# Kernel optimization log

Hardware: AMD Instinct MI355X
Metric: run time of the kernel (lower is better)

## Reference

```python
import jax, jax.numpy as jnp
import numpy as np

C, W = 144, 9225          # channel_count, batch_width
KW, F = 10, 64            # kernel_width, fc_segment_length
H1 = 128                  # second layer out
CAT = 2 * C * F           # 18432 = C*F (fc) + (W-KW+1) (conv)


def setup_inputs() -> dict:
    key = jax.random.key(0)
    ks = jax.random.split(key, 9)
    s_fc = 1.0 / np.sqrt(W)
    s_cv = 1.0 / np.sqrt(C * KW)
    s_1 = 1.0 / np.sqrt(CAT)
    s_2 = 1.0 / np.sqrt(H1)
    return {
        "x":     jax.random.normal(ks[0], (C, W), jnp.float32),
        "Wfc":   jax.random.normal(ks[1], (C, F, W), jnp.float32) * s_fc,
        "bfc":   jax.random.normal(ks[2], (C, F), jnp.float32) * s_fc,
        "Kconv": jax.random.normal(ks[3], (C, KW), jnp.float32) * s_cv,
        "bconv": jax.random.normal(ks[4], (1,), jnp.float32) * s_cv,
        "W1":    jax.random.normal(ks[5], (H1, CAT), jnp.float32) * s_1,
        "b1":    jax.random.normal(ks[6], (H1,), jnp.float32) * s_1,
        "W2":    jax.random.normal(ks[7], (1, H1), jnp.float32) * s_2,
        "b2":    jax.random.normal(ks[8], (1,), jnp.float32) * s_2,
    }


def reference(x, Wfc, bfc, Kconv, bconv, W1, b1, W2, b2):
    # 144 per-channel Linear(W->F) fused into one batched GEMV (no ReLU on
    # these in the original forward, despite the docstring).
    fc_out = (jnp.einsum('cfw,cw->cf', Wfc, x) + bfc).reshape(-1)  # [C*F]
    # Conv2d(1,1,(C,KW)): kernel height == channel count -> 1D valid corr.
    conv = jax.lax.conv_general_dilated(
        x[None, None],            # [1,1,C,W]
        Kconv[None, None],        # [1,1,C,KW]
        window_strides=(1, 1), padding='VALID')[0, 0, 0] + bconv  # [W-KW+1]
    concatenated = jnp.concatenate([fc_out, conv])                # [CAT]
    second = jax.nn.relu(W1 @ concatenated + b1)                  # [H1]
    out = jax.nn.relu(W2 @ second + b2)                           # [1]
    return jax.nn.sigmoid(out)
```

## Files before the change

kernel.cpp:

```cpp
#include <hip/hip_runtime.h>
#include <math.h>

#define CC    144
#define WW    9225
#define KWW   10
#define FF    64
#define H1N   128
#define CONVN (WW - KWW + 1)
#define CFN   (CC * FF)
#define CATN  (CFN + CONVN)

__global__ __launch_bounds__(256) void k_front(
    const float* __restrict__ x,
    const float* __restrict__ Wfc,
    const float* __restrict__ bfc,
    const float* __restrict__ Kc,
    const float* __restrict__ bconv,
    float* __restrict__ concat)
{
    __shared__ float sm[CC * KWW];
    const int b   = blockIdx.x;
    const int tid = threadIdx.x;

    if (b < CFN) {
        const int c = b >> 6;
        const size_t base = (size_t)b * WW;
        const float* __restrict__ xr = x + (size_t)c * WW;
        const float* __restrict__ wr = Wfc + base;

        const int pro = (int)((4u - ((unsigned)(base & 3u))) & 3u);
        float acc = 0.f;
        if (tid < pro) acc += wr[tid] * xr[tid];

        const int rem  = WW - pro;
        const int nv   = rem >> 2;
        const int tail = rem & 3;
        const float4* __restrict__ wv = (const float4*)(wr + pro);

        for (int i = tid; i < nv; i += 256) {
            const float4 wq = wv[i];
            const int w0 = pro + (i << 2);
            acc += wq.x * xr[w0]     + wq.y * xr[w0 + 1]
                 + wq.z * xr[w0 + 2] + wq.w * xr[w0 + 3];
        }
        if (tid < tail) {
            const int w0 = pro + (nv << 2) + tid;
            acc += wr[w0] * xr[w0];
        }

        #pragma unroll
        for (int off = 32; off > 0; off >>= 1)
            acc += __shfl_xor(acc, off, 64);
        const int lane = tid & 63, wid = tid >> 6;
        if (lane == 0) sm[wid] = acc;
        __syncthreads();
        if (tid == 0)
            concat[b] = sm[0] + sm[1] + sm[2] + sm[3] + bfc[b];
    } else {
        for (int i = tid; i < CC * KWW; i += 256) sm[i] = Kc[i];
        __syncthreads();

        const int p = (b - CFN) * 256 + tid;
        float acc = bconv[0];
        for (int c = 0; c < CC; ++c) {
            const float* __restrict__ xr = x + (size_t)c * WW + p;
            const float* __restrict__ kr = sm + c * KWW;
            #pragma unroll
            for (int k = 0; k < KWW; ++k)
                acc = fmaf(xr[k], kr[k], acc);
        }
        concat[CFN + p] = acc;
    }
}

__global__ __launch_bounds__(256) void k_layer1(
    const float* __restrict__ W1,
    const float* __restrict__ b1,
    const float* __restrict__ concat,
    float* __restrict__ second)
{
    __shared__ float sm[4];
    const int h = blockIdx.x, tid = threadIdx.x;
    const float4* __restrict__ wr = (const float4*)(W1 + (size_t)h * CATN);
    const float4* __restrict__ cv = (const float4*)concat;

    float acc = 0.f;
    #pragma unroll 2
    for (int i = tid; i < CATN / 4; i += 256) {
        const float4 a = wr[i], q = cv[i];
        acc += a.x * q.x + a.y * q.y + a.z * q.z + a.w * q.w;
    }
    #pragma unroll
    for (int off = 32; off > 0; off >>= 1)
        acc += __shfl_xor(acc, off, 64);
    if ((tid & 63) == 0) sm[tid >> 6] = acc;
    __syncthreads();
    if (tid == 0)
        second[h] = fmaxf(sm[0] + sm[1] + sm[2] + sm[3] + b1[h], 0.f);
}

__global__ __launch_bounds__(128) void k_final(
    const float* __restrict__ second,
    const float* __restrict__ W2,
    const float* __restrict__ b2,
    float* __restrict__ out)
{
    __shared__ float sm[2];
    const int tid = threadIdx.x;
    float v = second[tid] * W2[tid];
    #pragma unroll
    for (int off = 32; off > 0; off >>= 1)
        v += __shfl_xor(v, off, 64);
    if ((tid & 63) == 0) sm[tid >> 6] = v;
    __syncthreads();
    if (tid == 0) {
        float z = sm[0] + sm[1] + b2[0];
        z = fmaxf(z, 0.f);
        out[0] = 1.f / (1.f + expf(-z));
    }
}

extern "C" void kernel_launch(void* const* d_in, const int* in_sizes, int n_in,
                              void* d_out, int out_size, void* d_ws, size_t ws_size,
                              hipStream_t stream) {
    const float* x     = (const float*)d_in[0];
    const float* Wfc   = (const float*)d_in[1];
    const float* bfc   = (const float*)d_in[2];
    const float* Kc    = (const float*)d_in[3];
    const float* bconv = (const float*)d_in[4];
    const float* W1    = (const float*)d_in[5];
    const float* b1    = (const float*)d_in[6];
    const float* W2    = (const float*)d_in[7];
    const float* b2    = (const float*)d_in[8];
    float* out = (float*)d_out;

    float* concat = (float*)d_ws;
    float* second = concat + CATN;

    k_front <<<CFN + (CONVN / 256), 256, 0, stream>>>(x, Wfc, bfc, Kc, bconv, concat);
    k_layer1<<<H1N,                 256, 0, stream>>>(W1, b1, concat, second);
    k_final <<<1,                   128, 0, stream>>>(second, W2, b2, out);
}
```

Before: 93.80 us.

## Add shifted aligned x copies, nontemporal weight loads, and split layer1 rows

A pre-pass kernel builds four copies of x, each shifted by 0-3 elements and padded, so every FC row can read x as aligned float4 vectors instead of scalar loads. Wfc and W1 are read with nontemporal loads to keep the streaming weights out of the cache. Layer1 is split into two half-row blocks per output to double the block count, and the bias/ReLU moves into the final kernel. This adds an extra kernel launch plus about 5 MB of copy traffic, and it relies on enough workspace, falling back to the old path if there is not.

```diff
diff --git a/kernel.cpp b/kernel.cpp
--- a/kernel.cpp
+++ b/kernel.cpp
@@ -9,13 +9,39 @@
 #define CONVN (WW - KWW + 1)
 #define CFN   (CC * FF)
 #define CATN  (CFN + CONVN)
-
-__global__ __launch_bounds__(256) void k_front(
+#define WP    9232
+#define NCPY4 (4 * CC * (WP / 4))
+
+typedef float f32x4 __attribute__((ext_vector_type(4)));
+
+__global__ __launch_bounds__(256) void k_mkcopies(
+    const float* __restrict__ x, float* __restrict__ xcopy)
+{
+    const int total = NCPY4;
+    for (int idx = blockIdx.x * 256 + threadIdx.x; idx < total;
+         idx += gridDim.x * 256) {
+        const int q  = idx % (WP / 4);
+        const int sc = idx / (WP / 4);
+        const int c  = sc % CC;
+        const int s  = sc / CC;
+        const int j0 = q * 4;
+        const float* __restrict__ xr = x + (size_t)c * WW;
+        float4 v;
+        v.x = (s + j0 + 0 < WW) ? xr[s + j0 + 0] : 0.f;
+        v.y = (s + j0 + 1 < WW) ? xr[s + j0 + 1] : 0.f;
+        v.z = (s + j0 + 2 < WW) ? xr[s + j0 + 2] : 0.f;
+        v.w = (s + j0 + 3 < WW) ? xr[s + j0 + 3] : 0.f;
+        ((float4*)(xcopy + (size_t)sc * WP))[q] = v;
+    }
+}
+
+__global__ __launch_bounds__(256) void k_front_v2(
     const float* __restrict__ x,
     const float* __restrict__ Wfc,
     const float* __restrict__ bfc,
     const float* __restrict__ Kc,
     const float* __restrict__ bconv,
+    const float* __restrict__ xcopy,
     float* __restrict__ concat)
 {
     __shared__ float sm[CC * KWW];
@@ -25,23 +51,24 @@
     if (b < CFN) {
         const int c = b >> 6;
         const size_t base = (size_t)b * WW;
+        const float* __restrict__ wr = Wfc + base;
         const float* __restrict__ xr = x + (size_t)c * WW;
-        const float* __restrict__ wr = Wfc + base;
-
         const int pro = (int)((4u - ((unsigned)(base & 3u))) & 3u);
+
         float acc = 0.f;
         if (tid < pro) acc += wr[tid] * xr[tid];
 
         const int rem  = WW - pro;
         const int nv   = rem >> 2;
         const int tail = rem & 3;
-        const float4* __restrict__ wv = (const float4*)(wr + pro);
+        const f32x4* __restrict__ wv = (const f32x4*)(wr + pro);
+        const f32x4* __restrict__ xv =
+            (const f32x4*)(xcopy + (size_t)(pro * CC + c) * WP);
 
         for (int i = tid; i < nv; i += 256) {
-            const float4 wq = wv[i];
-            const int w0 = pro + (i << 2);
-            acc += wq.x * xr[w0]     + wq.y * xr[w0 + 1]
-                 + wq.z * xr[w0 + 2] + wq.w * xr[w0 + 3];
+            const f32x4 wq = __builtin_nontemporal_load(wv + i);
+            const f32x4 xq = xv[i];
+            acc += wq.x * xq.x + wq.y * xq.y + wq.z * xq.z + wq.w * xq.w;
         }
         if (tid < tail) {
             const int w0 = pro + (nv << 2) + tid;
@@ -59,7 +86,6 @@
     } else {
         for (int i = tid; i < CC * KWW; i += 256) sm[i] = Kc[i];
         __syncthreads();
-
         const int p = (b - CFN) * 256 + tid;
         float acc = bconv[0];
         for (int c = 0; c < CC; ++c) {
@@ -73,19 +99,114 @@
     }
 }
 
-__global__ __launch_bounds__(256) void k_layer1(
+__global__ __launch_bounds__(256) void k_layer1_v2(
     const float* __restrict__ W1,
+    const float* __restrict__ concat,
+    float* __restrict__ partial)
+{
+    __shared__ float sm[4];
+    const int j = blockIdx.x, tid = threadIdx.x;
+    const int h = j >> 1, half = j & 1;
+    const f32x4* __restrict__ wr =
+        (const f32x4*)(W1 + (size_t)h * CATN + half * (CATN / 2));
+    const f32x4* __restrict__ cv =
+        (const f32x4*)(concat + half * (CATN / 2));
+
+    float acc = 0.f;
+    for (int i = tid; i < CATN / 8; i += 256) {
+        const f32x4 a = __builtin_nontemporal_load(wr + i);
+        const f32x4 q = cv[i];
+        acc += a.x * q.x + a.y * q.y + a.z * q.z + a.w * q.w;
+    }
+    #pragma unroll
+    for (int off = 32; off > 0; off >>= 1)
+        acc += __shfl_xor(acc, off, 64);
+    if ((tid & 63) == 0) sm[tid >> 6] = acc;
+    __syncthreads();
+    if (tid == 0)
+        partial[j] = sm[0] + sm[1] + sm[2] + sm[3];
+}
+
+__global__ __launch_bounds__(128) void k_final_v2(
+    const float* __restrict__ partial,
     const float* __restrict__ b1,
-    const float* __restrict__ concat,
-    float* __restrict__ second)
+    const float* __restrict__ W2,
+    const float* __restrict__ b2,
+    float* __restrict__ out)
+{
+    __shared__ float sm[2];
+    const int tid = threadIdx.x;
+    float v = fmaxf(partial[2 * tid] + partial[2 * tid + 1] + b1[tid], 0.f)
+              * W2[tid];
+    #pragma unroll
+    for (int off = 32; off > 0; off >>= 1)
+        v += __shfl_xor(v, off, 64);
+    if ((tid & 63) == 0) sm[tid >> 6] = v;
+    __syncthreads();
+    if (tid == 0) {
+        float z = sm[0] + sm[1] + b2[0];
+        z = fmaxf(z, 0.f);
+        out[0] = 1.f / (1.f + expf(-z));
+    }
+}
+
+__global__ __launch_bounds__(256) void k_front_v1(
+    const float* __restrict__ x, const float* __restrict__ Wfc,
+    const float* __restrict__ bfc, const float* __restrict__ Kc,
+    const float* __restrict__ bconv, float* __restrict__ concat)
+{
+    __shared__ float sm[CC * KWW];
+    const int b = blockIdx.x, tid = threadIdx.x;
+    if (b < CFN) {
+        const int c = b >> 6;
+        const size_t base = (size_t)b * WW;
+        const float* __restrict__ xr = x + (size_t)c * WW;
+        const float* __restrict__ wr = Wfc + base;
+        const int pro = (int)((4u - ((unsigned)(base & 3u))) & 3u);
+        float acc = 0.f;
+        if (tid < pro) acc += wr[tid] * xr[tid];
+        const int rem = WW - pro, nv = rem >> 2, tail = rem & 3;
+        const float4* __restrict__ wv = (const float4*)(wr + pro);
+        for (int i = tid; i < nv; i += 256) {
+            const float4 wq = wv[i];
+            const int w0 = pro + (i << 2);
+            acc += wq.x * xr[w0] + wq.y * xr[w0 + 1]
+                 + wq.z * xr[w0 + 2] + wq.w * xr[w0 + 3];
+        }
+        if (tid < tail) {
+            const int w0 = pro + (nv << 2) + tid;
+            acc += wr[w0] * xr[w0];
+        }
+        #pragma unroll
+        for (int off = 32; off > 0; off >>= 1)
+            acc += __shfl_xor(acc, off, 64);
+        if ((tid & 63) == 0) sm[tid >> 6] = acc;
+        __syncthreads();
+        if (tid == 0) concat[b] = sm[0] + sm[1] + sm[2] + sm[3] + bfc[b];
+    } else {
+        for (int i = tid; i < CC * KWW; i += 256) sm[i] = Kc[i];
+        __syncthreads();
+        const int p = (b - CFN) * 256 + tid;
+        float acc = bconv[0];
+        for (int c = 0; c < CC; ++c) {
+            const float* __restrict__ xr = x + (size_t)c * WW + p;
+            const float* __restrict__ kr = sm + c * KWW;
+            #pragma unroll
+            for (int k = 0; k < KWW; ++k) acc = fmaf(xr[k], kr[k], acc);
+        }
+        concat[CFN + p] = acc;
+    }
+}
+
+__global__ __launch_bounds__(256) void k_layer1_v1(
+    const float* __restrict__ W1, const float* __restrict__ b1,
+    const float* __restrict__ concat, float* __restrict__ second)
 {
     __shared__ float sm[4];
     const int h = blockIdx.x, tid = threadIdx.x;
     const float4* __restrict__ wr = (const float4*)(W1 + (size_t)h * CATN);
     const float4* __restrict__ cv = (const float4*)concat;
-
     float acc = 0.f;
-    #pragma unroll 2
     for (int i = tid; i < CATN / 4; i += 256) {
         const float4 a = wr[i], q = cv[i];
         acc += a.x * q.x + a.y * q.y + a.z * q.z + a.w * q.w;
@@ -99,11 +220,9 @@
         second[h] = fmaxf(sm[0] + sm[1] + sm[2] + sm[3] + b1[h], 0.f);
 }
 
-__global__ __launch_bounds__(128) void k_final(
-    const float* __restrict__ second,
-    const float* __restrict__ W2,
-    const float* __restrict__ b2,
-    float* __restrict__ out)
+__global__ __launch_bounds__(128) void k_final_v1(
+    const float* __restrict__ second, const float* __restrict__ W2,
+    const float* __restrict__ b2, float* __restrict__ out)
 {
     __shared__ float sm[2];
     const int tid = threadIdx.x;
@@ -114,8 +233,7 @@
     if ((tid & 63) == 0) sm[tid >> 6] = v;
     __syncthreads();
     if (tid == 0) {
-        float z = sm[0] + sm[1] + b2[0];
-        z = fmaxf(z, 0.f);
+        float z = fmaxf(sm[0] + sm[1] + b2[0], 0.f);
         out[0] = 1.f / (1.f + expf(-z));
     }
 }
@@ -135,9 +253,22 @@
     float* out = (float*)d_out;
 
     float* concat = (float*)d_ws;
-    float* second = concat + CATN;
-
-    k_front <<<CFN + (CONVN / 256), 256, 0, stream>>>(x, Wfc, bfc, Kc, bconv, concat);
-    k_layer1<<<H1N,                 256, 0, stream>>>(W1, b1, concat, second);
-    k_final <<<1,                   128, 0, stream>>>(second, W2, b2, out);
-}
+    const size_t need =
+        ((size_t)(CATN + 256) + (size_t)4 * CC * WP) * sizeof(float);
+
+    if (ws_size >= need) {
+        float* partial = concat + CATN;
+        float* xcopy   = concat + CATN + 256;
+        k_mkcopies <<<1024, 256, 0, stream>>>(x, xcopy);
+        k_front_v2 <<<CFN + (CONVN / 256), 256, 0, stream>>>(
+            x, Wfc, bfc, Kc, bconv, xcopy, concat);
+        k_layer1_v2<<<256, 256, 0, stream>>>(W1, concat, partial);
+        k_final_v2 <<<1, 128, 0, stream>>>(partial, b1, W2, b2, out);
+    } else {
+        float* second = concat + CATN;
+        k_front_v1 <<<CFN + (CONVN / 256), 256, 0, stream>>>(
+            x, Wfc, bfc, Kc, bconv, concat);
+        k_layer1_v1<<<H1N, 256, 0, stream>>>(W1, b1, concat, second);
+        k_final_v1 <<<1, 128, 0, stream>>>(second, W2, b2, out);
+    }
+}
```

New measurement: 115.8 us. 1.23x slower.

## Map one wave per FC row and split layer-1 GEMV rows in half

Applied to the files above, without the earlier changes.

The FC front end now assigns each of a block's four waves its own output row, so a block covers four rows. This drops the cross-wave LDS reduction and the __syncthreads, and cuts the block count fourfold. Layer 1 is split into two half-row blocks per output, giving 256 blocks instead of 128 to fill more CUs; the final kernel sums the halves and applies bias and ReLU. Each wave now streams a full 9225-element row alone, which may lower memory-level parallelism per row, partly offset by unroll 4.

```diff
diff --git a/kernel.cpp b/kernel.cpp
--- a/kernel.cpp
+++ b/kernel.cpp
@@ -9,8 +9,11 @@
 #define CONVN (WW - KWW + 1)
 #define CFN   (CC * FF)
 #define CATN  (CFN + CONVN)
+#define FCB   (CFN / 4)
 
-__global__ __launch_bounds__(256) void k_front(
+typedef float f32x4 __attribute__((ext_vector_type(4)));
+
+__global__ __launch_bounds__(256) void k_front_v3(
     const float* __restrict__ x,
     const float* __restrict__ Wfc,
     const float* __restrict__ bfc,
@@ -19,48 +22,49 @@
     float* __restrict__ concat)
 {
     __shared__ float sm[CC * KWW];
-    const int b   = blockIdx.x;
+    const int bid = blockIdx.x;
     const int tid = threadIdx.x;
 
-    if (b < CFN) {
-        const int c = b >> 6;
-        const size_t base = (size_t)b * WW;
+    if (bid < FCB) {
+        const int wave = tid >> 6;
+        const int lane = tid & 63;
+        const int r    = bid * 4 + wave;
+        const int c    = r >> 6;
+        const size_t base = (size_t)r * WW;
+        const float* __restrict__ wr = Wfc + base;
         const float* __restrict__ xr = x + (size_t)c * WW;
-        const float* __restrict__ wr = Wfc + base;
 
         const int pro = (int)((4u - ((unsigned)(base & 3u))) & 3u);
         float acc = 0.f;
-        if (tid < pro) acc += wr[tid] * xr[tid];
+        if (lane < pro) acc += wr[lane] * xr[lane];
 
         const int rem  = WW - pro;
         const int nv   = rem >> 2;
         const int tail = rem & 3;
-        const float4* __restrict__ wv = (const float4*)(wr + pro);
+        const f32x4* __restrict__ wv = (const f32x4*)(wr + pro);
 
-        for (int i = tid; i < nv; i += 256) {
-            const float4 wq = wv[i];
+        #pragma unroll 4
+        for (int i = lane; i < nv; i += 64) {
+            const f32x4 wq = wv[i];
             const int w0 = pro + (i << 2);
             acc += wq.x * xr[w0]     + wq.y * xr[w0 + 1]
                  + wq.z * xr[w0 + 2] + wq.w * xr[w0 + 3];
         }
-        if (tid < tail) {
-            const int w0 = pro + (nv << 2) + tid;
+        if (lane < tail) {
+            const int w0 = pro + (nv << 2) + lane;
             acc += wr[w0] * xr[w0];
         }
 
         #pragma unroll
         for (int off = 32; off > 0; off >>= 1)
             acc += __shfl_xor(acc, off, 64);
-        const int lane = tid & 63, wid = tid >> 6;
-        if (lane == 0) sm[wid] = acc;
-        __syncthreads();
-        if (tid == 0)
-            concat[b] = sm[0] + sm[1] + sm[2] + sm[3] + bfc[b];
+        if (lane == 0)
+            concat[r] = acc + bfc[r];
     } else {
         for (int i = tid; i < CC * KWW; i += 256) sm[i] = Kc[i];
         __syncthreads();
 
-        const int p = (b - CFN) * 256 + tid;
+        const int p = (bid - FCB) * 256 + tid;
         float acc = bconv[0];
         for (int c = 0; c < CC; ++c) {
             const float* __restrict__ xr = x + (size_t)c * WW + p;
@@ -73,21 +77,23 @@
     }
 }
 
-__global__ __launch_bounds__(256) void k_layer1(
+__global__ __launch_bounds__(256) void k_layer1_v2(
     const float* __restrict__ W1,
-    const float* __restrict__ b1,
     const float* __restrict__ concat,
-    float* __restrict__ second)
+    float* __restrict__ partial)
 {
     __shared__ float sm[4];
-    const int h = blockIdx.x, tid = threadIdx.x;
-    const float4* __restrict__ wr = (const float4*)(W1 + (size_t)h * CATN);
-    const float4* __restrict__ cv = (const float4*)concat;
+    const int j = blockIdx.x, tid = threadIdx.x;
+    const int h = j >> 1, half = j & 1;
+    const f32x4* __restrict__ wr =
+        (const f32x4*)(W1 + (size_t)h * CATN + half * (CATN / 2));
+    const f32x4* __restrict__ cv =
+        (const f32x4*)(concat + half * (CATN / 2));
 
     float acc = 0.f;
-    #pragma unroll 2
-    for (int i = tid; i < CATN / 4; i += 256) {
-        const float4 a = wr[i], q = cv[i];
+    for (int i = tid; i < CATN / 8; i += 256) {
+        const f32x4 a = wr[i];
+        const f32x4 q = cv[i];
         acc += a.x * q.x + a.y * q.y + a.z * q.z + a.w * q.w;
     }
     #pragma unroll
@@ -96,18 +102,20 @@
     if ((tid & 63) == 0) sm[tid >> 6] = acc;
     __syncthreads();
     if (tid == 0)
-        second[h] = fmaxf(sm[0] + sm[1] + sm[2] + sm[3] + b1[h], 0.f);
+        partial[j] = sm[0] + sm[1] + sm[2] + sm[3];
 }
 
-__global__ __launch_bounds__(128) void k_final(
-    const float* __restrict__ second,
+__global__ __launch_bounds__(128) void k_final_v2(
+    const float* __restrict__ partial,
+    const float* __restrict__ b1,
     const float* __restrict__ W2,
     const float* __restrict__ b2,
     float* __restrict__ out)
 {
     __shared__ float sm[2];
     const int tid = threadIdx.x;
-    float v = second[tid] * W2[tid];
+    float v = fmaxf(partial[2 * tid] + partial[2 * tid + 1] + b1[tid], 0.f)
+              * W2[tid];
     #pragma unroll
     for (int off = 32; off > 0; off >>= 1)
         v += __shfl_xor(v, off, 64);
@@ -134,10 +142,11 @@
     const float* b2    = (const float*)d_in[8];
     float* out = (float*)d_out;
 
-    float* concat = (float*)d_ws;
-    float* second = concat + CATN;
+    float* concat  = (float*)d_ws;
+    float* partial = concat + CATN;
 
-    k_front <<<CFN + (CONVN / 256), 256, 0, stream>>>(x, Wfc, bfc, Kc, bconv, concat);
-    k_layer1<<<H1N,                 256, 0, stream>>>(W1, b1, concat, second);
-    k_final <<<1,                   128, 0, stream>>>(second, W2, b2, out);
+    k_front_v3 <<<FCB + (CONVN / 256), 256, 0, stream>>>(
+        x, Wfc, bfc, Kc, bconv, concat);
+    k_layer1_v2<<<256, 256, 0, stream>>>(W1, concat, partial);
+    k_final_v2 <<<1, 128, 0, stream>>>(partial, b1, W2, b2, out);
 }
```

New measurement: 88.11 us. 1.06x faster.
